# Optimization experiments

Hardware: AMD Instinct MI355X
Metric: run time of the kernel (lower is better)

The kernel has to match this reference:

```python
import jax, jax.numpy as jnp
import numpy as np
from jax import lax

B, CIN, HID, COUT = 64, 256, 256, 10
MULTI, KS = 3, 3
TH = TW = 7      # template (kernel) input spatial size
SH = SW = 31     # search input spatial size
EPS = 1e-5
DN = ('NCHW', 'OIHW', 'NCHW')


def _conv(x, w):
    return lax.conv_general_dilated(x, w, (1, 1), 'VALID', dimension_numbers=DN)


def _bn(x, p):
    # p: [4, C] packed (gamma, beta, running_mean, running_var); inference-mode BN
    g, b, m, v = p[0], p[1], p[2], p[3]
    inv = g / jnp.sqrt(v + EPS)
    return x * inv[:, None, None] + (b - m * inv)[:, None, None]


def _dwxcorr(x, k):
    # per-sample depthwise cross-correlation via groups = B*C trick
    b, c, h, w = x.shape
    kh, kw = k.shape[2], k.shape[3]
    y = lax.conv_general_dilated(
        x.reshape(1, b * c, h, w), k.reshape(b * c, 1, kh, kw),
        (1, 1), 'VALID', dimension_numbers=DN, feature_group_count=b * c)
    return y.reshape(b, c, y.shape[2], y.shape[3])


def _multixcorr(search, kernel):
    # crop template feature to 5x5 / 3x3 / 1x1 sub-kernels, xcorr each,
    # center-crop outputs to the common (smallest) size, concat on channels
    kh = kernel.shape[2]
    feats = []
    for i in range(MULTI):
        kk = kernel[:, :, i:kh - i, i:kh - i]
        o = _dwxcorr(search, kk)
        if i > 0:
            o = o[:, :, i:o.shape[2] - i, i:o.shape[3] - i]
        feats.append(o)
    return jnp.concatenate(feats, axis=1)  # [B, MULTI*HID, 25, 25]


def setup_inputs() -> dict:
    key = jax.random.key(0)
    ks = jax.random.split(key, 12)
    f32 = jnp.float32
    return {
        'kernel': jax.random.normal(ks[0], (B, CIN, TH, TW), f32),
        'search': jax.random.normal(ks[1], (B, CIN, SH, SW), f32),
        'wk': jax.random.normal(ks[2], (HID, CIN, KS, KS), f32) * 0.05,
        'bnk': jax.random.uniform(ks[3], (4, HID), f32, 0.1, 1.0),
        'ws': jax.random.normal(ks[4], (HID, CIN, KS, KS), f32) * 0.05,
        'bns': jax.random.uniform(ks[5], (4, HID), f32, 0.1, 1.0),
        'wd': jax.random.normal(ks[6], (HID, CIN * MULTI, 1, 1), f32) * 0.05,
        'bnd': jax.random.uniform(ks[7], (4, HID), f32, 0.1, 1.0),
        'wh1': jax.random.normal(ks[8], (HID, HID, 1, 1), f32) * 0.05,
        'bnh': jax.random.uniform(ks[9], (4, HID), f32, 0.1, 1.0),
        'wh2': jax.random.normal(ks[10], (COUT, HID, 1, 1), f32) * 0.05,
        'bh2': jax.random.normal(ks[11], (COUT,), f32) * 0.05,
    }


def reference(kernel, search, wk, bnk, ws, bns, wd, bnd, wh1, bnh, wh2, bh2):
    k = jax.nn.relu(_bn(_conv(kernel, wk), bnk))   # [B, HID, 5, 5]
    s = jax.nn.relu(_bn(_conv(search, ws), bns))   # [B, HID, 29, 29]
    feature = _multixcorr(s, k)                    # [B, 3*HID, 25, 25]
    feature = _bn(_conv(feature, wd), bnd)         # [B, HID, 25, 25]
    h = jax.nn.relu(_bn(_conv(feature, wh1), bnh))
    out = _conv(h, wh2) + bh2[:, None, None]       # [B, COUT, 25, 25]
    return out
```

## Files before the change

### kernel.cpp

```cpp
#include <hip/hip_runtime.h>
#include <hip/hip_bf16.h>
#include <cstdint>
#include <cstddef>

#define EPSBN 1e-5f

typedef unsigned short u16;
typedef unsigned int u32;
typedef _Float16 f16;
typedef _Float16 f16x8 __attribute__((ext_vector_type(8)));
typedef float f32x4 __attribute__((ext_vector_type(4)));

__device__ __forceinline__ void async_copy16(void* lds, const void* g) {
    __builtin_amdgcn_global_load_lds(
        (const __attribute__((address_space(1))) u32*)g,
        (__attribute__((address_space(3))) u32*)lds, 16, 0, 0);
}

__global__ __launch_bounds__(256) void prep_all(
    const float* __restrict__ sin, f16* __restrict__ sa,
    const float* __restrict__ kin, f16* __restrict__ ka,
    const float* __restrict__ wk, const float* __restrict__ ws,
    const float* __restrict__ wd, const float* __restrict__ wh1,
    const float* __restrict__ wh2, f16* __restrict__ bpk,
    f16* __restrict__ bps, f16* __restrict__ bpd, f16* __restrict__ bp1,
    f16* __restrict__ bp2) {
    __shared__ float tile[64][65];
    int t = blockIdx.x;
    int tid = threadIdx.x;
    if (t < 4352) {
        int b = t / 68;
        int rem = t - b * 68;
        int c0 = (rem / 17) * 64;
        int z = rem % 17;
        bool isk = (z == 16);
        const float* in = isk ? kin : sin;
        f16* op = isk ? ka : sa;
        int HW = isk ? 49 : 961;
        int h0 = isk ? 0 : z * 64;
        int cl = tid >> 6;
        int hl = tid & 63;
        for (int r = cl; r < 64; r += 4) {
            int hw = h0 + hl;
            tile[r][hl] =
                (hw < HW) ? in[(size_t)(b * 256 + c0 + r) * HW + hw] : 0.f;
        }
        __syncthreads();
        int c = tid & 63;
        for (int r = cl; r < 64; r += 4) {
            int hw = h0 + r;
            if (hw < HW)
                op[((size_t)b * HW + hw) * 256 + c0 + c] = (f16)tile[c][r];
        }
        return;
    }
    int blk = t - 4352;
    const float* W;
    f16* Bp;
    int nK32, OCr, K, i;
    bool conv = false;
    if (blk < 2304) {
        W = wk; Bp = bpk; nK32 = 72; OCr = 256; K = 2304; conv = true;
        i = blk * 256 + tid;
    } else if (blk < 4608) {
        W = ws; Bp = bps; nK32 = 72; OCr = 256; K = 2304; conv = true;
        i = (blk - 2304) * 256 + tid;
    } else if (blk < 5376) {
        W = wd; Bp = bpd; nK32 = 24; OCr = 256; K = 768;
        i = (blk - 4608) * 256 + tid;
    } else if (blk < 5632) {
        W = wh1; Bp = bp1; nK32 = 8; OCr = 256; K = 256;
        i = (blk - 5376) * 256 + tid;
    } else {
        W = wh2; Bp = bp2; nK32 = 8; OCr = 10; K = 256;
        i = (blk - 5632) * 256 + tid;
    }
    int per = nK32 * 512;
    int oct = i / per;
    int r = i - oct * per;
    int k32 = r >> 9;
    int lr = r & 511;
    int l = lr >> 3, j = lr & 7;
    int oc = oct * 16 + (l & 15);
    int k = k32 * 32 + ((l >> 4) << 3) + j;
    float v = 0.f;
    if (oc < OCr)
        v = conv ? W[(size_t)(oc * 256 + (k & 255)) * 9 + (k >> 8)]
                 : W[(size_t)oc * K + k];
    Bp[(size_t)(oct * nK32 + k32) * 512 + lr] = (f16)v;
}

template <int KHW, int EPI>
__device__ __forceinline__ void gemm_body(
    f16* sA, const f16* __restrict__ A, const f16* __restrict__ Bp,
    const float* __restrict__ bnp, float* __restrict__ outF,
    f16* __restrict__ oF, int m0, int n0, int M, int OC, int C, int H, int W,
    int OH, int OW) {
    const int Ktot = KHW * C;
    const int nKb = Ktot >> 7;
    const int nK32 = Ktot >> 5;
    const int tid = threadIdx.x;
    const int OHW = OH * OW;

    int abase[8];
#pragma unroll
    for (int s = 0; s < 8; ++s) {
        int idx = tid + s * 256;
        int ml = idx >> 4;
        int qs = (idx & 15) ^ (ml & 15);
        int m = m0 + ml;
        if (m >= M) m = M - 1;
        int b = m / OHW;
        int r = m - b * OHW;
        int y = r / OW;
        int x = r - y * OW;
        abase[s] = ((b * H + y) * W + x) * C + qs * 8;
    }

    f32x4 acc[4][4];
#pragma unroll
    for (int i = 0; i < 4; ++i)
#pragma unroll
        for (int j = 0; j < 4; ++j) acc[i][j] = (f32x4)0.f;

    const int lane = tid & 63;
    const int row = lane & 15;
    const int quad = lane >> 4;
    const int wv = tid >> 6;
    const int wm = (wv & 1) * 64;
    const int wn = (wv >> 1) * 64;
    const int octb = (n0 + wn) >> 4;

    for (int kb = 0; kb < nKb; ++kb) {
        int koff;
        if (KHW == 9) {
            int pos = kb >> 1;
            int cin0 = (kb & 1) << 7;
            int ky = pos / 3;
            int kx = pos - ky * 3;
            koff = (ky * W + kx) * C + cin0;
        } else {
            koff = kb << 7;
        }
#pragma unroll
        for (int s = 0; s < 8; ++s)
            async_copy16(&sA[tid * 8 + s * 2048], A + abase[s] + koff);

        f16x8 bh[4][4];
#pragma unroll
        for (int ks = 0; ks < 4; ++ks)
#pragma unroll
            for (int j = 0; j < 4; ++j)
                bh[ks][j] = *(const f16x8*)&Bp[((size_t)(octb + j) * nK32 +
                                               kb * 4 + ks) *
                                                  512 +
                                              lane * 8];
        __syncthreads();

#pragma unroll
        for (int ks = 0; ks < 4; ++ks) {
            f16x8 ah[4];
#pragma unroll
            for (int i = 0; i < 4; ++i) {
                int g = wm + i * 16 + row;
                ah[i] =
                    *(const f16x8*)&sA[g * 128 +
                                       ((((ks << 2) | quad) ^ row) << 3)];
            }
#pragma unroll
            for (int i = 0; i < 4; ++i)
#pragma unroll
                for (int j = 0; j < 4; ++j)
                    acc[i][j] = __builtin_amdgcn_mfma_f32_16x16x32_f16(
                        ah[i], bh[ks][j], acc[i][j], 0, 0, 0);
        }
        __syncthreads();
    }

#pragma unroll
    for (int j = 0; j < 4; ++j) {
        int oc = n0 + wn + j * 16 + row;
        bool ocv = oc < OC;
        float scale = 1.f, shift = 0.f;
        if (ocv) {
            if (EPI != 3) {
                float g = bnp[oc];
                float bb = bnp[OC + oc];
                float mm = bnp[2 * OC + oc];
                float vv = bnp[3 * OC + oc];
                float inv = g * rsqrtf(vv + EPSBN);
                scale = inv;
                shift = bb - mm * inv;
            } else {
                shift = bnp[oc];
            }
        }
#pragma unroll
        for (int i = 0; i < 4; ++i) {
#pragma unroll
            for (int r = 0; r < 4; ++r) {
                int m = m0 + wm + i * 16 + quad * 4 + r;
                if (m < M && ocv) {
                    float v = acc[i][j][r] * scale + shift;
                    if (EPI == 2) v = fmaxf(v, 0.f);
                    if (EPI == 3) {
                        int b = m / OHW;
                        int rr = m - b * OHW;
                        outF[((size_t)b * OC + oc) * OHW + rr] = v;
                    } else {
                        oF[(size_t)m * OC + oc] = (f16)v;
                    }
                }
            }
        }
    }
}

__global__ __launch_bounds__(256, 3) void conv33_fused(
    const f16* sA_g, const f16* bpS, const float* bns, f16* sOut,
    const f16* kA_g, const f16* bpK, const float* bnk, f16* kOut) {
    __shared__ f16 sA[16384];
    bool sec = blockIdx.x >= 421;
    const f16* A = sec ? kA_g : sA_g;
    const f16* Bp = sec ? bpK : bpS;
    const float* bnp = sec ? bnk : bns;
    f16* oF = sec ? kOut : sOut;
    int M = sec ? 1600 : 53824;
    int H = sec ? 7 : 31;
    int OHs = sec ? 5 : 29;
    int m0 = (blockIdx.x - (sec ? 421 : 0)) * 128;
    int n0 = blockIdx.y * 128;
    gemm_body<9, 2>(sA, A, Bp, bnp, nullptr, oF, m0, n0, M, 256, 256, H, H,
                    OHs, OHs);
}

template <int EPI>
__global__ __launch_bounds__(256, 3) void gemm_1x1(
    const f16* __restrict__ A, const f16* __restrict__ Bp,
    const float* __restrict__ bnp, float* __restrict__ outF,
    f16* __restrict__ oF, int M, int OC, int C) {
    __shared__ f16 sA[16384];
    gemm_body<1, EPI>(sA, A, Bp, bnp, outF, oF, blockIdx.x * 128,
                      blockIdx.y * 128, M, OC, C, 25, 25, 25, 25);
}

__global__ __launch_bounds__(256) void xcorr_nhwc(
    const f16* __restrict__ sf, const f16* __restrict__ kf,
    f16* __restrict__ feat) {
    int by = blockIdx.x;
    int b = by / 25;
    int y = by - b * 25;
    int c = threadIdx.x;
    float kv[25];
#pragma unroll
    for (int p = 0; p < 25; ++p)
        kv[p] = (float)kf[(size_t)(b * 25 + p) * 256 + c];
    const f16* srow = sf + (size_t)(b * 29 + y) * 29 * 256 + c;
    float sv[25];
#pragma unroll
    for (int d = 0; d < 5; ++d)
#pragma unroll
        for (int e = 0; e < 5; ++e)
            sv[d * 5 + e] = (float)srow[(size_t)(d * 29 + e) * 256];
    for (int x = 0;; ++x) {
        float a0 = 0.f, a1 = 0.f, a2;
#pragma unroll
        for (int p = 0; p < 25; ++p) a0 = fmaf(sv[p], kv[p], a0);
#pragma unroll
        for (int d = 1; d < 4; ++d)
#pragma unroll
            for (int e = 1; e < 4; ++e)
                a1 = fmaf(sv[d * 5 + e], kv[d * 5 + e], a1);
        a2 = sv[12] * kv[12];
        size_t o = ((size_t)by * 25 + x) * 768 + c;
        feat[o] = (f16)a0;
        feat[o + 256] = (f16)a1;
        feat[o + 512] = (f16)a2;
        if (x == 24) break;
#pragma unroll
        for (int d = 0; d < 5; ++d) {
#pragma unroll
            for (int e = 0; e < 4; ++e) sv[d * 5 + e] = sv[d * 5 + e + 1];
            sv[d * 5 + 4] = (float)srow[(size_t)(d * 29 + x + 5) * 256];
        }
    }
}

extern "C" void kernel_launch(void* const* d_in, const int* in_sizes, int n_in,
                              void* d_out, int out_size, void* d_ws,
                              size_t ws_size, hipStream_t stream) {
    const float* kernel_in = (const float*)d_in[0];
    const float* search_in = (const float*)d_in[1];
    const float* wk = (const float*)d_in[2];
    const float* bnk = (const float*)d_in[3];
    const float* ws = (const float*)d_in[4];
    const float* bns = (const float*)d_in[5];
    const float* wd = (const float*)d_in[6];
    const float* bnd = (const float*)d_in[7];
    const float* wh1 = (const float*)d_in[8];
    const float* bnh = (const float*)d_in[9];
    const float* wh2 = (const float*)d_in[10];
    const float* bh2 = (const float*)d_in[11];
    float* out = (float*)d_out;

    char* base = (char*)d_ws;
    size_t off = 0;
    auto alloc = [&](size_t bytes) {
        off = (off + 511) & ~(size_t)511;
        void* p = base + off;
        off += bytes;
        return p;
    };

    f16* bpd = (f16*)alloc((size_t)16 * 24 * 512 * 2);
    f16* bp1 = (f16*)alloc((size_t)16 * 8 * 512 * 2);
    f16* bp2 = (f16*)alloc((size_t)8 * 8 * 512 * 2);
    size_t Pf = (off + 511) & ~(size_t)511;
    f16* kfeat = (f16*)alloc((size_t)1600 * 256 * 2);
    f16* sfeat = (f16*)alloc((size_t)53824 * 256 * 2);
    size_t P1 = (off + 511) & ~(size_t)511;
    f16* bpk = (f16*)alloc((size_t)16 * 72 * 512 * 2);
    f16* bps = (f16*)alloc((size_t)16 * 72 * 512 * 2);
    f16* ka = (f16*)alloc((size_t)64 * 49 * 256 * 2);
    f16* sa = (f16*)alloc((size_t)64 * 961 * 256 * 2);
    f16* feat = (f16*)(base + P1);
    f16* f2 = (f16*)(base + Pf);
    f16* hb = (f16*)(base + P1);

    prep_all<<<dim3(10112), 256, 0, stream>>>(search_in, sa, kernel_in, ka,
                                              wk, ws, wd, wh1, wh2, bpk, bps,
                                              bpd, bp1, bp2);
    conv33_fused<<<dim3(434, 2), 256, 0, stream>>>(sa, bps, bns, sfeat, ka,
                                                   bpk, bnk, kfeat);
    xcorr_nhwc<<<dim3(1600), 256, 0, stream>>>(sfeat, kfeat, feat);
    gemm_1x1<1><<<dim3(313, 2), 256, 0, stream>>>(feat, bpd, bnd, nullptr, f2,
                                                  40000, 256, 768);
    gemm_1x1<2><<<dim3(313, 2), 256, 0, stream>>>(f2, bp1, bnh, nullptr, hb,
                                                  40000, 256, 256);
    gemm_1x1<3><<<dim3(313, 1), 256, 0, stream>>>(hb, bp2, bh2, out, nullptr,
                                                  40000, 10, 256);
}
```

Measured before the change: 332.3 us.

## Double-buffer A tiles and B registers in GEMM main loop

Measured after the change: 330.2 us. About the same (-0.6%).

```diff
diff --git a/kernel.cpp b/kernel.cpp
--- a/kernel.cpp
+++ b/kernel.cpp
@@ -131,41 +131,43 @@
     const int wn = (wv >> 1) * 64;
     const int octb = (n0 + wn) >> 4;
 
-    for (int kb = 0; kb < nKb; ++kb) {
-        int koff;
+    auto koff_of = [&](int kb) {
         if (KHW == 9) {
             int pos = kb >> 1;
             int cin0 = (kb & 1) << 7;
             int ky = pos / 3;
             int kx = pos - ky * 3;
-            koff = (ky * W + kx) * C + cin0;
-        } else {
-            koff = kb << 7;
-        }
+            return (ky * W + kx) * C + cin0;
+        }
+        return kb << 7;
+    };
+    auto issueA = [&](int bufbase, int kb) {
+        int koff = koff_of(kb);
 #pragma unroll
         for (int s = 0; s < 8; ++s)
-            async_copy16(&sA[tid * 8 + s * 2048], A + abase[s] + koff);
-
-        f16x8 bh[4][4];
+            async_copy16(&sA[bufbase + tid * 8 + s * 2048],
+                         A + abase[s] + koff);
+    };
+    auto loadB = [&](f16x8(&bh)[4][4], int kb) {
 #pragma unroll
         for (int ks = 0; ks < 4; ++ks)
 #pragma unroll
             for (int j = 0; j < 4; ++j)
-                bh[ks][j] = *(const f16x8*)&Bp[((size_t)(octb + j) * nK32 +
-                                               kb * 4 + ks) *
-                                                  512 +
-                                              lane * 8];
-        __syncthreads();
-
+                bh[ks][j] =
+                    *(const f16x8*)&Bp[((size_t)(octb + j) * nK32 + kb * 4 +
+                                        ks) *
+                                           512 +
+                                       lane * 8];
+    };
+    auto compute = [&](int bufbase, f16x8(&bh)[4][4]) {
 #pragma unroll
         for (int ks = 0; ks < 4; ++ks) {
             f16x8 ah[4];
 #pragma unroll
             for (int i = 0; i < 4; ++i) {
                 int g = wm + i * 16 + row;
-                ah[i] =
-                    *(const f16x8*)&sA[g * 128 +
-                                       ((((ks << 2) | quad) ^ row) << 3)];
+                ah[i] = *(const f16x8*)&sA[bufbase + g * 128 +
+                                           ((((ks << 2) | quad) ^ row) << 3)];
             }
 #pragma unroll
             for (int i = 0; i < 4; ++i)
@@ -174,7 +176,22 @@
                     acc[i][j] = __builtin_amdgcn_mfma_f32_16x16x32_f16(
                         ah[i], bh[ks][j], acc[i][j], 0, 0, 0);
         }
+    };
+
+    f16x8 bh0[4][4], bh1[4][4];
+    issueA(0, 0);
+    loadB(bh0, 0);
+    for (int kb = 0; kb < nKb; kb += 2) {
         __syncthreads();
+        issueA(16384, kb + 1);
+        loadB(bh1, kb + 1);
+        compute(0, bh0);
+        __syncthreads();
+        if (kb + 2 < nKb) {
+            issueA(0, kb + 2);
+            loadB(bh0, kb + 2);
+        }
+        compute(16384, bh1);
     }
 
 #pragma unroll
@@ -216,11 +233,11 @@
     }
 }
 
-__global__ __launch_bounds__(256, 3) void conv33_fused(
+__global__ __launch_bounds__(256, 2) void conv33_fused(
     const f16* sA_g, const f16* bpS, const float* bns, f16* sOut,
     const f16* kA_g, const f16* bpK, const float* bnk, f16* kOut) {
-    __shared__ f16 sA[16384];
-    bool sec = blockIdx.x >= 421;
+    __shared__ f16 sA[32768];
+    bool sec = blockIdx.x < 13;
     const f16* A = sec ? kA_g : sA_g;
     const f16* Bp = sec ? bpK : bpS;
     const float* bnp = sec ? bnk : bns;
@@ -228,18 +245,18 @@
     int M = sec ? 1600 : 53824;
     int H = sec ? 7 : 31;
     int OHs = sec ? 5 : 29;
-    int m0 = (blockIdx.x - (sec ? 421 : 0)) * 128;
+    int m0 = (sec ? blockIdx.x : (blockIdx.x - 13)) * 128;
     int n0 = blockIdx.y * 128;
     gemm_body<9, 2>(sA, A, Bp, bnp, nullptr, oF, m0, n0, M, 256, 256, H, H,
                     OHs, OHs);
 }
 
 template <int EPI>
-__global__ __launch_bounds__(256, 3) void gemm_1x1(
+__global__ __launch_bounds__(256, 2) void gemm_1x1(
     const f16* __restrict__ A, const f16* __restrict__ Bp,
     const float* __restrict__ bnp, float* __restrict__ outF,
     f16* __restrict__ oF, int M, int OC, int C) {
-    __shared__ f16 sA[16384];
+    __shared__ f16 sA[32768];
     gemm_body<1, EPI>(sA, A, Bp, bnp, outF, oF, blockIdx.x * 128,
                       blockIdx.y * 128, M, OC, C, 25, 25, 25, 25);
 }
```
